# Kernel tuning notes

Measured on AMD Instinct MI355X. Metric: run time of the kernel, lower is better.

The kernel has to match this reference:

```python
import jax, jax.numpy as jnp
import numpy as np

NUM_HEADS = 16
D_MODEL = 1024
HEAD_DIM = D_MODEL // NUM_HEADS  # 64
NEG_INF = -1e9


def alibi_bidirectional_bias(num_heads, seq_len, dtype=jnp.float32):
    """[num_heads, S, S] bias: first H/2 heads forward-causal ALiBi, last H/2 backward."""
    half = num_heads // 2
    base = 24.0 ** (1.0 / half)
    slopes = (1.0 / base ** jnp.arange(1, half + 1, dtype=dtype))[:, None, None]  # [half,1,1]
    pos = jnp.arange(seq_len)
    rel = (pos[None, :] - pos[:, None]).astype(dtype)  # rel[i,j] = j - i
    neg = jnp.full((seq_len, seq_len), NEG_INF, dtype=dtype)
    fwd = slopes * jnp.tril(rel) + jnp.triu(neg, 1)          # causal (attend past)
    bwd = slopes * jnp.triu(-rel) + jnp.tril(neg, -1)        # anti-causal (attend future)
    return jnp.concatenate([fwd, bwd], axis=0)  # [H, S, S]


def setup_inputs() -> dict:
    key = jax.random.key(0)
    ks = jax.random.split(key, 9)
    B, S, D = 2, 2048, D_MODEL
    sc = 1.0 / np.sqrt(D)
    inp = {"x": jax.random.normal(ks[0], (B, S, D), dtype=jnp.float32)}
    inp["Wq"] = jax.random.normal(ks[1], (D, D), dtype=jnp.float32) * sc
    inp["bq"] = jnp.zeros((D,), dtype=jnp.float32)
    inp["Wk"] = jax.random.normal(ks[2], (D, D), dtype=jnp.float32) * sc
    inp["bk"] = jnp.zeros((D,), dtype=jnp.float32)
    inp["Wv"] = jax.random.normal(ks[3], (D, D), dtype=jnp.float32) * sc
    inp["bv"] = jnp.zeros((D,), dtype=jnp.float32)
    inp["Wf"] = jax.random.normal(ks[4], (D, D), dtype=jnp.float32) * sc
    inp["bf"] = jnp.zeros((D,), dtype=jnp.float32)
    return inp


def reference(x, Wq, bq, Wk, bk, Wv, bv, Wf, bf):
    B, S, D = x.shape
    H, hd = NUM_HEADS, HEAD_DIM

    def heads(y):  # [B,S,D] -> [B,H,S,hd]
        return y.reshape(B, S, H, hd).transpose(0, 2, 1, 3)

    q = heads(x @ Wq + bq)
    k = heads(x @ Wk + bk)
    v = heads(x @ Wv + bv)

    bias = alibi_bidirectional_bias(H, S, x.dtype)  # [H,S,S]
    scores = jnp.einsum("bhqd,bhkd->bhqk", q, k) * (1.0 / np.sqrt(hd)) + bias[None]
    attn = jax.nn.softmax(scores, axis=-1)
    out = jnp.einsum("bhqk,bhkd->bhqd", attn, v)
    out = out.transpose(0, 2, 1, 3).reshape(B, S, D)
    return out @ Wf + bf
```

## Files before the change

### kernel.cpp

```cpp
#include <hip/hip_runtime.h>

#define S_LEN 2048
#define NH 16
#define HD 64
#define DM 1024
#define BSZ 2

typedef __bf16 bf16;
typedef __bf16 bf16x8 __attribute__((ext_vector_type(8)));
typedef float f32x4 __attribute__((ext_vector_type(4)));
typedef const unsigned int __attribute__((address_space(1)))* gas_ptr;
typedef unsigned int __attribute__((address_space(3)))* las_ptr;

__device__ __forceinline__ void gl_lds16(const bf16* g, bf16* l) {
  __builtin_amdgcn_global_load_lds((gas_ptr)g, (las_ptr)l, 16, 0, 0);
}

__global__ __launch_bounds__(256) void k_cast(const float* __restrict__ in,
                                              bf16* __restrict__ out, int n4) {
  int i = blockIdx.x * 256 + threadIdx.x;
  if (i >= n4) return;
  float4 v = ((const float4*)in)[i];
  union { ushort4 u; bf16 b[4]; } o;
  o.b[0] = (bf16)v.x; o.b[1] = (bf16)v.y; o.b[2] = (bf16)v.z; o.b[3] = (bf16)v.w;
  ((ushort4*)out)[i] = o.u;
}

__global__ __launch_bounds__(256) void k_transpose_w4(
    const float* __restrict__ W0, const float* __restrict__ W1,
    const float* __restrict__ W2, const float* __restrict__ W3,
    bf16* __restrict__ dqkv, bf16* __restrict__ df) {
  __shared__ float t[64][65];
  const int z = blockIdx.z;
  const float* W = (z == 0) ? W0 : (z == 1) ? W1 : (z == 2) ? W2 : W3;
  bf16* D = (z < 3) ? (dqkv + (size_t)z * 1048576) : df;
  int k0 = blockIdx.x * 64, n0 = blockIdx.y * 64;
  int c = threadIdx.x & 63, rr = threadIdx.x >> 6;
#pragma unroll
  for (int it = 0; it < 16; ++it) {
    int r = it * 4 + rr;
    t[r][c] = W[(size_t)(k0 + r) * DM + n0 + c];
  }
  __syncthreads();
#pragma unroll
  for (int it = 0; it < 16; ++it) {
    int r = it * 4 + rr;
    D[(size_t)(n0 + r) * DM + k0 + c] = (bf16)t[c][r];
  }
}

template <int MODE, int BM, int BN>
__global__ __launch_bounds__(256) void k_gemm(
    const bf16* __restrict__ A, const bf16* __restrict__ Bt,
    const float* __restrict__ b0, const float* __restrict__ b1,
    const float* __restrict__ b2, void* __restrict__ Cout,
    bf16* __restrict__ VtOut, int M, int N, int K) {
  __shared__ __align__(16) bf16 As[BM * 64];
  __shared__ __align__(16) bf16 Bs[BN * 64];
  constexpr int MIc = BM / 32, NIc = BN / 32;
  const int tid = threadIdx.x;
  const int l = tid & 63, w = tid >> 6;
  const int lm = l & 15, lg = l >> 4;
  const int bm = blockIdx.x * BM, bn = blockIdx.y * BN;
  const int wm = (w >> 1) * (BM / 2), wn = (w & 1) * (BN / 2);

  f32x4 acc[MIc][NIc] = {};
  const bf16* Ag = A + (size_t)bm * K;
  const bf16* Bg = Bt + (size_t)bn * K;

  for (int k0 = 0; k0 < K; k0 += 64) {
#pragma unroll
    for (int it = 0; it < BM / 32; ++it) {
      int cl = it * 256 + tid;
      int row = cl >> 3;
      int cs = ((cl & 7) ^ (row & 7)) << 3;
      gl_lds16(Ag + (size_t)row * K + k0 + cs, &As[(it * 256 + w * 64) * 8]);
    }
#pragma unroll
    for (int it = 0; it < BN / 32; ++it) {
      int cl = it * 256 + tid;
      int row = cl >> 3;
      int cs = ((cl & 7) ^ (row & 7)) << 3;
      gl_lds16(Bg + (size_t)row * K + k0 + cs, &Bs[(it * 256 + w * 64) * 8]);
    }
    __syncthreads();
#pragma unroll
    for (int kk = 0; kk < 2; ++kk) {
      bf16x8 af[MIc], bfr[NIc];
#pragma unroll
      for (int mi = 0; mi < MIc; ++mi) {
        int row = wm + mi * 16 + lm;
        af[mi] = *(const bf16x8*)&As[row * 64 + ((((kk << 2) + lg) ^ (row & 7)) << 3)];
      }
#pragma unroll
      for (int ni = 0; ni < NIc; ++ni) {
        int row = wn + ni * 16 + lm;
        bfr[ni] = *(const bf16x8*)&Bs[row * 64 + ((((kk << 2) + lg) ^ (row & 7)) << 3)];
      }
#pragma unroll
      for (int mi = 0; mi < MIc; ++mi)
#pragma unroll
        for (int ni = 0; ni < NIc; ++ni)
          acc[mi][ni] = __builtin_amdgcn_mfma_f32_16x16x32_bf16(
              af[mi], bfr[ni], acc[mi][ni], 0, 0, 0);
    }
    __syncthreads();
  }

#pragma unroll
  for (int ni = 0; ni < NIc; ++ni) {
    int n = bn + wn + ni * 16 + lm;
    float bv;
    if (MODE == 0) {
      const float* bp = (n < 1024) ? b0 : (n < 2048) ? b1 : b2;
      bv = bp[n & 1023];
    } else {
      bv = b0[n];
    }
#pragma unroll
    for (int mi = 0; mi < MIc; ++mi) {
#pragma unroll
      for (int r = 0; r < 4; ++r) {
        int m = bm + wm + mi * 16 + lg * 4 + r;
        float v = acc[mi][ni][r] + bv;
        if (MODE == 0) {
          int qkv = n >> 10;
          int h = (n >> 6) & 15;
          int d = n & 63;
          int b = m >> 11, s = m & 2047;
          if (qkv == 2) {
            VtOut[((size_t)(b * NH + h) * HD + d) * S_LEN + s] = (bf16)v;
          } else {
            ((bf16*)Cout)[(size_t)qkv * (BSZ * NH * S_LEN * HD) +
                          ((size_t)(b * NH + h) * S_LEN + s) * HD + d] = (bf16)v;
          }
        } else {
          ((float*)Cout)[(size_t)m * N + n] = v;
        }
      }
    }
  }
}

#define SMX(MASKED)                                                           \
  {                                                                           \
    const float t0 = slp2 * (float)dlo;                                       \
    _Pragma("unroll") for (int ni = 0; ni < 4; ++ni) {                        \
      const int koff = (ni & 1) * 32 + (ni >> 1) * 4;                         \
      float bni = t0 + dni[ni];                                               \
      float pr[4];                                                            \
      _Pragma("unroll") for (int r = 0; r < 4; ++r) {                         \
        float v = fmaf(sc[ni][r], c1, bni + srr[r]);                          \
        if (MASKED) {                                                         \
          int reli = dlo + koff + relc + r;                                   \
          bool ok = causal ? (reli <= 0) : (reli >= 0);                       \
          v = ok ? v : -1e9f;                                                 \
        }                                                                     \
        pr[r] = __builtin_amdgcn_exp2f(v);                                    \
      }                                                                       \
      union { bf16 b[2]; unsigned u; } u0, u1;                                \
      u0.b[0] = (bf16)pr[0]; u0.b[1] = (bf16)pr[1];                           \
      u1.b[0] = (bf16)pr[2]; u1.b[1] = (bf16)pr[3];                           \
      pk[ni][0] = u0.u; pk[ni][1] = u1.u;                                     \
    }                                                                         \
  }

__global__ __launch_bounds__(512, 2) void k_attn(const bf16* __restrict__ Qh,
                                                 const bf16* __restrict__ Kh,
                                                 const bf16* __restrict__ Vt,
                                                 bf16* __restrict__ O) {
  __shared__ __align__(16) bf16 Ks[2][4096];
  __shared__ __align__(16) bf16 Vs[2][4096];
  const int id = blockIdx.x;
  const int bh = ((id & 7) << 2) | ((id >> 3) & 3);
  const int pid = id >> 5;
  const int b = bh >> 4, h = bh & 15;
  const bool causal = (h < 8);
  const int tid = threadIdx.x;
  const int w = tid >> 6, l = tid & 63;
  const int lm = l & 15, lg = l >> 4;
  const int hh = causal ? h : h - 8;
  const float c1 = 0.18033688f;
  const float sm = __builtin_amdgcn_exp2f(-(float)(hh + 1) * 0.57312035f) * 1.44269504f;
  const float slp2 = causal ? sm : -sm;
  const int relc = lg * 8 - lm;
  const int krow_lane = ((lm >> 2) << 3) + (lm & 3);
  const int swzK = (lm & 3) | (((lm >> 2) & 1) << 2);
  const int swzV = (lm & 3) | (((lm >> 3) & 1) << 2);
  float dni[4], srr[4];
#pragma unroll
  for (int ni = 0; ni < 4; ++ni)
    dni[ni] = slp2 * (float)((ni & 1) * 32 + (ni >> 1) * 4);
#pragma unroll
  for (int r = 0; r < 4; ++r) srr[r] = slp2 * (float)(relc + r);

  const bf16* Qp = Qh + (size_t)bh * S_LEN * HD;
  const bf16* Kp = Kh + (size_t)bh * S_LEN * HD;
  const bf16* Vp = Vt + (size_t)bh * HD * S_LEN;

  bf16x8 ones;
#pragma unroll
  for (int i = 0; i < 8; ++i) ones[i] = (bf16)1.0f;

  auto stage = [&](bf16* lk, bf16* lv, int j0) {
    const int row = tid >> 3, c = tid & 7;
    const int sw = (row & 3) | (((row >> 3) & 1) << 2);
    const int gc = (c ^ sw) << 3;
    const int clb8 = ((tid >> 6) << 6) * 8;
    gl_lds16(Kp + (size_t)(j0 + row) * HD + gc, lk + clb8);
    gl_lds16(Vp + (size_t)row * S_LEN + j0 + gc, lv + clb8);
  };

  auto run_strip = [&](int yi) {
    const int qb = yi << 7;
    const int q0 = qb + w * 16;
    const int jbase = causal ? 0 : qb;
    const int jcnt = causal ? (qb >> 6) + 2 : ((S_LEN - qb) >> 6);

    bf16x8 qf[2];
#pragma unroll
    for (int kk = 0; kk < 2; ++kk)
      qf[kk] = *(const bf16x8*)&Qp[(size_t)(q0 + lm) * HD + kk * 32 + lg * 8];

    f32x4 oacc[4] = {};
    f32x4 lacc = {};

    stage(Ks[0], Vs[0], jbase);
    __syncthreads();

    for (int t = 0; t < jcnt; ++t) {
      const int cur = t & 1;
      if (t + 1 < jcnt) stage(Ks[cur ^ 1], Vs[cur ^ 1], jbase + (t + 1) * 64);
      const int j0 = jbase + t * 64;
      const int dlo = j0 - q0;
      const bool skip = causal ? (dlo >= 16) : (dlo <= -64);
      if (!skip) {
        const bf16* lk = Ks[cur];
        const bf16* lv = Vs[cur];
        f32x4 sc[4] = {};
#pragma unroll
        for (int kk = 0; kk < 2; ++kk)
#pragma unroll
          for (int ni = 0; ni < 4; ++ni) {
            const int koff = (ni & 1) * 32 + (ni >> 1) * 4;
            bf16x8 kf = *(const bf16x8*)&lk[(koff + krow_lane) * 64 +
                                            ((((kk << 2) + lg) ^ swzK) << 3)];
            sc[ni] = __builtin_amdgcn_mfma_f32_16x16x32_bf16(kf, qf[kk], sc[ni],
                                                             0, 0, 0);
          }
        bf16x8 vf[2][4];
#pragma unroll
        for (int kk = 0; kk < 2; ++kk)
#pragma unroll
          for (int di = 0; di < 4; ++di)
            vf[kk][di] = *(const bf16x8*)&lv[(di * 16 + lm) * 64 +
                                             ((((kk << 2) + lg) ^ swzV) << 3)];
        const bool full = causal ? (dlo <= -63) : (dlo >= 15);
        unsigned pk[4][2];
        if (full) { SMX(false); } else { SMX(true); }
#pragma unroll
        for (int kk = 0; kk < 2; ++kk) {
          union { unsigned d[4]; bf16x8 v; } pa;
          pa.d[0] = pk[kk][0];
          pa.d[1] = pk[kk][1];
          pa.d[2] = pk[kk + 2][0];
          pa.d[3] = pk[kk + 2][1];
          lacc = __builtin_amdgcn_mfma_f32_16x16x32_bf16(pa.v, ones, lacc, 0, 0, 0);
#pragma unroll
          for (int di = 0; di < 4; ++di)
            oacc[di] = __builtin_amdgcn_mfma_f32_16x16x32_bf16(pa.v, vf[kk][di],
                                                               oacc[di], 0, 0, 0);
        }
      }
      __syncthreads();
    }

    float rin[4];
#pragma unroll
    for (int r = 0; r < 4; ++r) rin[r] = 1.0f / lacc[r];
#pragma unroll
    for (int di = 0; di < 4; ++di) {
      int d = h * HD + di * 16 + lm;
#pragma unroll
      for (int r = 0; r < 4; ++r) {
        int q = q0 + lg * 4 + r;
        O[((size_t)b * S_LEN + q) * DM + d] = (bf16)(oacc[di][r] * rin[r]);
      }
    }
  };

  run_strip(pid);
  run_strip(15 - pid);
}

extern "C" void kernel_launch(void* const* d_in, const int* in_sizes, int n_in,
                              void* d_out, int out_size, void* d_ws, size_t ws_size,
                              hipStream_t stream) {
  const float* x  = (const float*)d_in[0];
  const float* Wq = (const float*)d_in[1];
  const float* bq = (const float*)d_in[2];
  const float* Wk = (const float*)d_in[3];
  const float* bk = (const float*)d_in[4];
  const float* Wv = (const float*)d_in[5];
  const float* bv = (const float*)d_in[6];
  const float* Wf = (const float*)d_in[7];
  const float* bfp = (const float*)d_in[8];

  char* ws = (char*)d_ws;
  const size_t MB = 1ull << 20;
  bf16* xb    = (bf16*)(ws);
  bf16* Wqkvt = (bf16*)(ws + 8 * MB);
  bf16* Wft   = (bf16*)(ws + 14 * MB);
  bf16* QKVh  = (bf16*)(ws + 16 * MB);
  bf16* Vt    = (bf16*)(ws + 40 * MB);
  bf16* O     = QKVh + 2 * 4194304;

  k_cast<<<4096, 256, 0, stream>>>(x, xb, 1048576);
  k_transpose_w4<<<dim3(16, 16, 4), 256, 0, stream>>>(Wq, Wk, Wv, Wf, Wqkvt, Wft);
  k_gemm<0, 128, 128><<<dim3(32, 24), 256, 0, stream>>>(
      xb, Wqkvt, bq, bk, bv, QKVh, Vt, 4096, 3072, 1024);
  k_attn<<<256, 512, 0, stream>>>(QKVh, QKVh + 4194304, Vt, O);
  k_gemm<2, 64, 128><<<dim3(64, 8), 256, 0, stream>>>(
      O, Wft, bfp, bfp, bfp, d_out, nullptr, 4096, 1024, 1024);
}
```

Baseline: 189.7 us.

## Merge cast and weight-transpose kernels; use explicit vmcnt waits in attention pipeline

Merges the input cast and weight transpose into one k_prep launch, removing one kernel launch and its gap. In the attention kernel, the double-buffered K/V loop now uses explicit s_waitcnt vmcnt(2) plus raw s_barrier instead of __syncthreads. This lets the prefetch of the next tile stay in flight while the current tile is computed, instead of draining all loads at every barrier. The risk is correctness: the vmcnt count must match the number of outstanding global_load_lds operations per thread.

```diff
diff --git a/kernel.cpp b/kernel.cpp
--- a/kernel.cpp
+++ b/kernel.cpp
@@ -16,25 +16,28 @@
   __builtin_amdgcn_global_load_lds((gas_ptr)g, (las_ptr)l, 16, 0, 0);
 }
 
-__global__ __launch_bounds__(256) void k_cast(const float* __restrict__ in,
-                                              bf16* __restrict__ out, int n4) {
-  int i = blockIdx.x * 256 + threadIdx.x;
-  if (i >= n4) return;
-  float4 v = ((const float4*)in)[i];
-  union { ushort4 u; bf16 b[4]; } o;
-  o.b[0] = (bf16)v.x; o.b[1] = (bf16)v.y; o.b[2] = (bf16)v.z; o.b[3] = (bf16)v.w;
-  ((ushort4*)out)[i] = o.u;
-}
-
-__global__ __launch_bounds__(256) void k_transpose_w4(
+#define CFENCE asm volatile("" ::: "memory")
+
+__global__ __launch_bounds__(256) void k_prep(
+    const float* __restrict__ x, bf16* __restrict__ xb,
     const float* __restrict__ W0, const float* __restrict__ W1,
     const float* __restrict__ W2, const float* __restrict__ W3,
     bf16* __restrict__ dqkv, bf16* __restrict__ df) {
   __shared__ float t[64][65];
-  const int z = blockIdx.z;
+  const int id = blockIdx.x;
+  if (id < 4096) {
+    int i = id * 256 + threadIdx.x;
+    float4 v = ((const float4*)x)[i];
+    union { ushort4 u; bf16 b[4]; } o;
+    o.b[0] = (bf16)v.x; o.b[1] = (bf16)v.y; o.b[2] = (bf16)v.z; o.b[3] = (bf16)v.w;
+    ((ushort4*)xb)[i] = o.u;
+    return;
+  }
+  const int id2 = id - 4096;
+  const int z = id2 >> 8;
   const float* W = (z == 0) ? W0 : (z == 1) ? W1 : (z == 2) ? W2 : W3;
   bf16* D = (z < 3) ? (dqkv + (size_t)z * 1048576) : df;
-  int k0 = blockIdx.x * 64, n0 = blockIdx.y * 64;
+  int k0 = ((id2 >> 4) & 15) * 64, n0 = (id2 & 15) * 64;
   int c = threadIdx.x & 63, rr = threadIdx.x >> 6;
 #pragma unroll
   for (int it = 0; it < 16; ++it) {
@@ -225,55 +228,70 @@
     f32x4 oacc[4] = {};
     f32x4 lacc = {};
 
-    stage(Ks[0], Vs[0], jbase);
-    __syncthreads();
-
-    for (int t = 0; t < jcnt; ++t) {
-      const int cur = t & 1;
-      if (t + 1 < jcnt) stage(Ks[cur ^ 1], Vs[cur ^ 1], jbase + (t + 1) * 64);
+    auto compute = [&](int t, const bf16* lk, const bf16* lv) {
       const int j0 = jbase + t * 64;
       const int dlo = j0 - q0;
       const bool skip = causal ? (dlo >= 16) : (dlo <= -64);
-      if (!skip) {
-        const bf16* lk = Ks[cur];
-        const bf16* lv = Vs[cur];
-        f32x4 sc[4] = {};
-#pragma unroll
-        for (int kk = 0; kk < 2; ++kk)
-#pragma unroll
-          for (int ni = 0; ni < 4; ++ni) {
-            const int koff = (ni & 1) * 32 + (ni >> 1) * 4;
-            bf16x8 kf = *(const bf16x8*)&lk[(koff + krow_lane) * 64 +
-                                            ((((kk << 2) + lg) ^ swzK) << 3)];
-            sc[ni] = __builtin_amdgcn_mfma_f32_16x16x32_bf16(kf, qf[kk], sc[ni],
-                                                             0, 0, 0);
-          }
-        bf16x8 vf[2][4];
-#pragma unroll
-        for (int kk = 0; kk < 2; ++kk)
-#pragma unroll
-          for (int di = 0; di < 4; ++di)
-            vf[kk][di] = *(const bf16x8*)&lv[(di * 16 + lm) * 64 +
-                                             ((((kk << 2) + lg) ^ swzV) << 3)];
-        const bool full = causal ? (dlo <= -63) : (dlo >= 15);
-        unsigned pk[4][2];
-        if (full) { SMX(false); } else { SMX(true); }
-#pragma unroll
-        for (int kk = 0; kk < 2; ++kk) {
-          union { unsigned d[4]; bf16x8 v; } pa;
-          pa.d[0] = pk[kk][0];
-          pa.d[1] = pk[kk][1];
-          pa.d[2] = pk[kk + 2][0];
-          pa.d[3] = pk[kk + 2][1];
-          lacc = __builtin_amdgcn_mfma_f32_16x16x32_bf16(pa.v, ones, lacc, 0, 0, 0);
-#pragma unroll
-          for (int di = 0; di < 4; ++di)
-            oacc[di] = __builtin_amdgcn_mfma_f32_16x16x32_bf16(pa.v, vf[kk][di],
-                                                               oacc[di], 0, 0, 0);
+      if (skip) return;
+      f32x4 sc[4] = {};
+#pragma unroll
+      for (int kk = 0; kk < 2; ++kk)
+#pragma unroll
+        for (int ni = 0; ni < 4; ++ni) {
+          const int koff = (ni & 1) * 32 + (ni >> 1) * 4;
+          bf16x8 kf = *(const bf16x8*)&lk[(koff + krow_lane) * 64 +
+                                          ((((kk << 2) + lg) ^ swzK) << 3)];
+          sc[ni] = __builtin_amdgcn_mfma_f32_16x16x32_bf16(kf, qf[kk], sc[ni],
+                                                           0, 0, 0);
         }
-      }
-      __syncthreads();
-    }
+      bf16x8 vf[2][4];
+#pragma unroll
+      for (int kk = 0; kk < 2; ++kk)
+#pragma unroll
+        for (int di = 0; di < 4; ++di)
+          vf[kk][di] = *(const bf16x8*)&lv[(di * 16 + lm) * 64 +
+                                           ((((kk << 2) + lg) ^ swzV) << 3)];
+      const bool full = causal ? (dlo <= -63) : (dlo >= 15);
+      unsigned pk[4][2];
+      if (full) { SMX(false); } else { SMX(true); }
+#pragma unroll
+      for (int kk = 0; kk < 2; ++kk) {
+        union { unsigned d[4]; bf16x8 v; } pa;
+        pa.d[0] = pk[kk][0];
+        pa.d[1] = pk[kk][1];
+        pa.d[2] = pk[kk + 2][0];
+        pa.d[3] = pk[kk + 2][1];
+        lacc = __builtin_amdgcn_mfma_f32_16x16x32_bf16(pa.v, ones, lacc, 0, 0, 0);
+#pragma unroll
+        for (int di = 0; di < 4; ++di)
+          oacc[di] = __builtin_amdgcn_mfma_f32_16x16x32_bf16(pa.v, vf[kk][di],
+                                                             oacc[di], 0, 0, 0);
+      }
+    };
+
+    stage(Ks[0], Vs[0], jbase);
+    asm volatile("s_waitcnt vmcnt(0)" ::: "memory");
+    __builtin_amdgcn_s_barrier();
+    CFENCE;
+
+    for (int t = 0; t < jcnt - 1; ++t) {
+      const int cur = t & 1;
+      stage(Ks[cur ^ 1], Vs[cur ^ 1], jbase + (t + 1) * 64);
+      asm volatile("s_waitcnt vmcnt(2)" ::: "memory");
+      __builtin_amdgcn_s_barrier();
+      CFENCE;
+      compute(t, Ks[cur], Vs[cur]);
+      CFENCE;
+      __builtin_amdgcn_s_barrier();
+      CFENCE;
+    }
+    asm volatile("s_waitcnt vmcnt(0)" ::: "memory");
+    __builtin_amdgcn_s_barrier();
+    CFENCE;
+    compute(jcnt - 1, Ks[(jcnt - 1) & 1], Vs[(jcnt - 1) & 1]);
+    CFENCE;
+    __builtin_amdgcn_s_barrier();
+    CFENCE;
 
     float rin[4];
 #pragma unroll
@@ -315,8 +333,7 @@
   bf16* Vt    = (bf16*)(ws + 40 * MB);
   bf16* O     = QKVh + 2 * 4194304;
 
-  k_cast<<<4096, 256, 0, stream>>>(x, xb, 1048576);
-  k_transpose_w4<<<dim3(16, 16, 4), 256, 0, stream>>>(Wq, Wk, Wv, Wf, Wqkvt, Wft);
+  k_prep<<<5120, 256, 0, stream>>>(x, xb, Wq, Wk, Wv, Wf, Wqkvt, Wft);
   k_gemm<0, 128, 128><<<dim3(32, 24), 256, 0, stream>>>(
       xb, Wqkvt, bq, bk, bv, QKVh, Vt, 4096, 3072, 1024);
   k_attn<<<256, 512, 0, stream>>>(QKVh, QKVh + 4194304, Vt, O);
```

Result: no change. 186.1 us (-1.9%).
